# Kernel optimization log

Hardware: AMD Instinct MI355X
Metric: run time of the kernel (lower is better)

## Reference

```python
import jax, jax.numpy as jnp
import numpy as np

NUM_HEADS = 16
D_MODEL = 1024
DEPTH = D_MODEL // NUM_HEADS


def setup_inputs() -> dict:
    key = jax.random.key(0)
    ks = jax.random.split(key, 9)
    B, S = 2, 2048
    scale = 1.0 / np.sqrt(D_MODEL)
    return {
        "x": jax.random.normal(ks[0], (B, S, D_MODEL), dtype=jnp.float32),
        "wq": jax.random.normal(ks[1], (D_MODEL, D_MODEL), dtype=jnp.float32) * scale,
        "bq": jnp.zeros((D_MODEL,), dtype=jnp.float32),
        "wk": jax.random.normal(ks[2], (D_MODEL, D_MODEL), dtype=jnp.float32) * scale,
        "bk": jnp.zeros((D_MODEL,), dtype=jnp.float32),
        "wv": jax.random.normal(ks[3], (D_MODEL, D_MODEL), dtype=jnp.float32) * scale,
        "bv": jnp.zeros((D_MODEL,), dtype=jnp.float32),
        "wo": jax.random.normal(ks[4], (D_MODEL, D_MODEL), dtype=jnp.float32) * scale,
        "bo": jnp.zeros((D_MODEL,), dtype=jnp.float32),
    }


def _split_heads(t):
    # [B, S, D] -> [B, H, S, depth]
    B, S, _ = t.shape
    return t.reshape(B, S, NUM_HEADS, DEPTH).transpose(0, 2, 1, 3)


def reference(x, wq, bq, wk, bk, wv, bv, wo, bo):
    q = _split_heads(x @ wq + bq)  # [B,H,S,d]
    k = _split_heads(x @ wk + bk)
    v = _split_heads(x @ wv + bv)
    logits = jnp.einsum("bhqd,bhkd->bhqk", q, k) / jnp.sqrt(jnp.float32(DEPTH))
    attn = jax.nn.softmax(logits, axis=-1)  # [B,H,S,S]
    ctx = jnp.einsum("bhqk,bhkd->bhqd", attn, v)
    B, H, S, d = ctx.shape
    concat = ctx.transpose(0, 2, 1, 3).reshape(B, S, D_MODEL)
    out = concat @ wo + bo
    return out, attn
```

## Files before the change

### kernel.cpp

```cpp
#include <hip/hip_runtime.h>
#include <hip/hip_bf16.h>

#define SEQ 2048
#define BATCH 2
#define NH 16
#define DM 1024
#define DEPTH 64
#define MROWS (BATCH * SEQ)

typedef __attribute__((ext_vector_type(8))) short bf16x8;
typedef __attribute__((ext_vector_type(4))) float f32x4;

__device__ __forceinline__ float b2f(ushort u) {
    union { uint i; float f; } v; v.i = ((uint)u) << 16; return v.f;
}
__device__ __forceinline__ ushort f2b(float f) {
    __hip_bfloat16 h = __float2bfloat16(f);
    return *reinterpret_cast<ushort*>(&h);
}

__device__ __forceinline__ void gload_lds16(const void* g, void* l) {
    __builtin_amdgcn_global_load_lds((const __attribute__((address_space(1))) void*)g,
                                     (__attribute__((address_space(3))) void*)l, 16, 0, 0);
}

__global__ __launch_bounds__(256) void convert_f32_bf16(const float* __restrict__ in,
                                                        ushort* __restrict__ outp, int n4) {
    int i = blockIdx.x * 256 + threadIdx.x;
    if (i < n4) {
        const float4 v = ((const float4*)in)[i];
        ushort4 o;
        o.x = f2b(v.x); o.y = f2b(v.y); o.z = f2b(v.z); o.w = f2b(v.w);
        ((ushort4*)outp)[i] = o;
    }
}

__global__ __launch_bounds__(256) void transpose_convert4(const float* __restrict__ w0,
                                                          const float* __restrict__ w1,
                                                          const float* __restrict__ w2,
                                                          const float* __restrict__ w3,
                                                          ushort* __restrict__ WtBase) {
    __shared__ float tile[32][33];
    const int z = blockIdx.z;
    const float* W = (z == 0) ? w0 : (z == 1) ? w1 : (z == 2) ? w2 : w3;
    ushort* Wt = WtBase + (size_t)z * DM * DM;
    const int bx = blockIdx.x * 32;
    const int by = blockIdx.y * 32;
    const int tx = threadIdx.x & 31, ty = threadIdx.x >> 5;
#pragma unroll
    for (int i = 0; i < 32; i += 8)
        tile[ty + i][tx] = W[(size_t)(by + ty + i) * DM + bx + tx];
    __syncthreads();
#pragma unroll
    for (int i = 0; i < 32; i += 8)
        Wt[(size_t)(bx + ty + i) * DM + by + tx] = f2b(tile[tx][ty + i]);
}

__global__ __launch_bounds__(256) void gemm_qkv_mfma(const ushort* __restrict__ A,
                                                     const ushort* __restrict__ WtAll,
                                                     const float* __restrict__ bq,
                                                     const float* __restrict__ bk,
                                                     const float* __restrict__ bv,
                                                     ushort* __restrict__ OutBase) {
    __shared__ __align__(16) ushort As[128 * 32];
    __shared__ __align__(16) ushort Bs[128 * 32];

    const int t    = threadIdx.x;
    const int lane = t & 63;
    const int w    = t >> 6;
    const int wr   = w >> 1, wc = w & 1;
    const int row0 = blockIdx.y * 128;
    const int col0 = blockIdx.x * 128;
    const int bank = col0 >> 10;
    const float* bias = (bank == 0) ? bq : (bank == 1) ? bk : bv;
    const float scale = (bank == 0) ? 0.125f : 1.0f;
    const int ccol0 = col0 & 1023;
    ushort* Cout = OutBase + (size_t)bank * MROWS * DM;

    f32x4 acc[4][4];
#pragma unroll
    for (int mi = 0; mi < 4; ++mi)
#pragma unroll
        for (int ni = 0; ni < 4; ++ni) acc[mi][ni] = (f32x4){0.f, 0.f, 0.f, 0.f};

    const int sr = t >> 2;
    const int sc = (t & 3) * 8;

    for (int k0 = 0; k0 < DM; k0 += 32) {
        gload_lds16(&A[(size_t)(row0 + sr) * DM + k0 + sc],          &As[w * 512]);
        gload_lds16(&A[(size_t)(row0 + 64 + sr) * DM + k0 + sc],     &As[2048 + w * 512]);
        gload_lds16(&WtAll[(size_t)(col0 + sr) * DM + k0 + sc],      &Bs[w * 512]);
        gload_lds16(&WtAll[(size_t)(col0 + 64 + sr) * DM + k0 + sc], &Bs[2048 + w * 512]);
        __syncthreads();

        bf16x8 af[4], bfr[4];
#pragma unroll
        for (int mi = 0; mi < 4; ++mi)
            af[mi] = *(const bf16x8*)&As[(wr * 64 + mi * 16 + (lane & 15)) * 32 + (lane >> 4) * 8];
#pragma unroll
        for (int ni = 0; ni < 4; ++ni)
            bfr[ni] = *(const bf16x8*)&Bs[(wc * 64 + ni * 16 + (lane & 15)) * 32 + (lane >> 4) * 8];
#pragma unroll
        for (int mi = 0; mi < 4; ++mi)
#pragma unroll
            for (int ni = 0; ni < 4; ++ni)
                acc[mi][ni] = __builtin_amdgcn_mfma_f32_16x16x32_bf16(af[mi], bfr[ni], acc[mi][ni], 0, 0, 0);
        __syncthreads();
    }

    float bb[4];
#pragma unroll
    for (int ni = 0; ni < 4; ++ni) bb[ni] = bias[ccol0 + wc * 64 + ni * 16 + (lane & 15)];

#pragma unroll
    for (int mi = 0; mi < 4; ++mi) {
        const int row = row0 + wr * 64 + mi * 16 + (lane >> 4) * 4;
#pragma unroll
        for (int ni = 0; ni < 4; ++ni) {
            const int col = ccol0 + wc * 64 + ni * 16 + (lane & 15);
#pragma unroll
            for (int r = 0; r < 4; ++r)
                Cout[(size_t)(row + r) * DM + col] = f2b((acc[mi][ni][r] + bb[ni]) * scale);
        }
    }
}

__global__ __launch_bounds__(256) void gemm_mfma_f32(const ushort* __restrict__ A,
                                                     const ushort* __restrict__ Wt,
                                                     const float* __restrict__ bias,
                                                     float* __restrict__ Cout) {
    __shared__ __align__(16) ushort As[128 * 32];
    __shared__ __align__(16) ushort Bs[128 * 32];

    const int t    = threadIdx.x;
    const int lane = t & 63;
    const int w    = t >> 6;
    const int wr   = w >> 1, wc = w & 1;
    const int row0 = blockIdx.y * 128;
    const int col0 = blockIdx.x * 128;

    f32x4 acc[4][4];
#pragma unroll
    for (int mi = 0; mi < 4; ++mi)
#pragma unroll
        for (int ni = 0; ni < 4; ++ni) acc[mi][ni] = (f32x4){0.f, 0.f, 0.f, 0.f};

    const int sr = t >> 2;
    const int sc = (t & 3) * 8;

    for (int k0 = 0; k0 < DM; k0 += 32) {
        gload_lds16(&A[(size_t)(row0 + sr) * DM + k0 + sc],       &As[w * 512]);
        gload_lds16(&A[(size_t)(row0 + 64 + sr) * DM + k0 + sc],  &As[2048 + w * 512]);
        gload_lds16(&Wt[(size_t)(col0 + sr) * DM + k0 + sc],      &Bs[w * 512]);
        gload_lds16(&Wt[(size_t)(col0 + 64 + sr) * DM + k0 + sc], &Bs[2048 + w * 512]);
        __syncthreads();

        bf16x8 af[4], bfr[4];
#pragma unroll
        for (int mi = 0; mi < 4; ++mi)
            af[mi] = *(const bf16x8*)&As[(wr * 64 + mi * 16 + (lane & 15)) * 32 + (lane >> 4) * 8];
#pragma unroll
        for (int ni = 0; ni < 4; ++ni)
            bfr[ni] = *(const bf16x8*)&Bs[(wc * 64 + ni * 16 + (lane & 15)) * 32 + (lane >> 4) * 8];
#pragma unroll
        for (int mi = 0; mi < 4; ++mi)
#pragma unroll
            for (int ni = 0; ni < 4; ++ni)
                acc[mi][ni] = __builtin_amdgcn_mfma_f32_16x16x32_bf16(af[mi], bfr[ni], acc[mi][ni], 0, 0, 0);
        __syncthreads();
    }

    float bb[4];
#pragma unroll
    for (int ni = 0; ni < 4; ++ni) bb[ni] = bias[col0 + wc * 64 + ni * 16 + (lane & 15)];

#pragma unroll
    for (int mi = 0; mi < 4; ++mi) {
        const int row = row0 + wr * 64 + mi * 16 + (lane >> 4) * 4;
#pragma unroll
        for (int ni = 0; ni < 4; ++ni) {
            const int col = col0 + wc * 64 + ni * 16 + (lane & 15);
#pragma unroll
            for (int r = 0; r < 4; ++r)
                Cout[(size_t)(row + r) * DM + col] = acc[mi][ni][r] + bb[ni];
        }
    }
}

__global__ __launch_bounds__(256) void transpose_v(const ushort* __restrict__ Vh,
                                                   ushort* __restrict__ Vt3) {
    __shared__ ushort tile[64][80];
    const int t  = threadIdx.x;
    const int bh = blockIdx.x;
    const int cc = blockIdx.y;
    const int k0 = cc * 64;
    const int b  = bh >> 4;
    const int h  = bh & 15;
    const size_t panel = (size_t)b * SEQ * DM + (size_t)h * DEPTH;

    {
        const int k = t >> 2, dc = (t & 3) * 16;
        const ushort* src = Vh + panel + (size_t)(k0 + k) * DM + dc;
        *(bf16x8*)&tile[k][dc]     = *(const bf16x8*)src;
        *(bf16x8*)&tile[k][dc + 8] = *(const bf16x8*)(src + 8);
    }
    __syncthreads();
    {
        const int l  = t & 63;
        const int ni = t >> 6;
        const int kr = (l >> 4) * 8;
        const int dl = ni * 16 + (l & 15);
#pragma unroll
        for (int kh = 0; kh < 2; ++kh) {
            bf16x8 o;
#pragma unroll
            for (int j = 0; j < 8; ++j) o[j] = tile[kh * 32 + kr + j][dl];
            char* dst = (char*)Vt3 +
                        (((size_t)bh * 64 + cc * 2 + kh) * 4 + ni) * 1024 + l * 16;
            *(bf16x8*)dst = o;
        }
    }
}

__global__ __launch_bounds__(256) void transpose_k(const ushort* __restrict__ Kh,
                                                   ushort* __restrict__ Kf) {
    __shared__ ushort tile[64][80];
    const int t  = threadIdx.x;
    const int bh = blockIdx.x;
    const int cc = blockIdx.y;
    const int k0 = cc * 64;
    const int b  = bh >> 4;
    const int h  = bh & 15;
    const size_t panel = (size_t)b * SEQ * DM + (size_t)h * DEPTH;

    {
        const int k = t >> 2, dc = (t & 3) * 16;
        const ushort* src = Kh + panel + (size_t)(k0 + k) * DM + dc;
        *(bf16x8*)&tile[k][dc]     = *(const bf16x8*)src;
        *(bf16x8*)&tile[k][dc + 8] = *(const bf16x8*)(src + 8);
    }
    __syncthreads();
    {
        const int l   = t & 63;
        const int sub = t >> 6;
        const int row = sub * 16 + (l & 15);
        const int db  = (l >> 4) * 8;
#pragma unroll
        for (int ks = 0; ks < 2; ++ks) {
            bf16x8 o;
#pragma unroll
            for (int j = 0; j < 8; ++j) o[j] = tile[row][ks * 32 + db + j];
            char* dst = (char*)Kf +
                        ((((size_t)bh * 128 + cc * 4 + sub) * 2) + ks) * 1024 + l * 16;
            *(bf16x8*)dst = o;
        }
    }
}

__global__ __launch_bounds__(512, 2) void attn_fused_kernel(const ushort* __restrict__ Qh,
                                                            const ushort* __restrict__ Kfrag,
                                                            const ushort* __restrict__ Vt3,
                                                            float* __restrict__ attn_out,
                                                            ushort* __restrict__ Ctx) {
    __shared__ __align__(16) ushort P_lds[16 * 2048];
    __shared__ float red[256];

    const int t    = threadIdx.x;
    const int lane = t & 63;
    const int w    = t >> 6;
    const int qt   = blockIdx.x;
    const int bh   = blockIdx.y;
    const int b    = bh >> 4;
    const int h    = bh & 15;
    const int q0   = qt * 16;
    const int q    = lane & 15;
    const int g    = lane >> 4;
    const int swzP = (q & 7) << 4;

    const size_t panel = (size_t)b * SEQ * DM + (size_t)h * DEPTH;
    char* Pb = (char*)P_lds;

    const ushort* Qrow = Qh + panel + (size_t)(q0 + q) * DM + g * 8;
    const bf16x8 qf0 = *(const bf16x8*)Qrow;
    const bf16x8 qf1 = *(const bf16x8*)(Qrow + 32);

    const char* Kf = (const char*)Kfrag + (size_t)bh * 262144;
    f32x4 acc[16];
#pragma unroll
    for (int i = 0; i < 16; ++i) acc[i] = (f32x4){0.f, 0.f, 0.f, 0.f};

#pragma unroll
    for (int i = 0; i < 16; ++i) {
        const char* fb = Kf + (size_t)((w * 16 + i) * 2) * 1024 + lane * 16;
        const bf16x8 kf0 = *(const bf16x8*)fb;
        const bf16x8 kf1 = *(const bf16x8*)(fb + 1024);
        acc[i] = __builtin_amdgcn_mfma_f32_16x16x32_bf16(kf0, qf0, acc[i], 0, 0, 0);
        acc[i] = __builtin_amdgcn_mfma_f32_16x16x32_bf16(kf1, qf1, acc[i], 0, 0, 0);
    }

    float mm = acc[0][0];
#pragma unroll
    for (int i = 0; i < 16; ++i) {
#pragma unroll
        for (int r = 0; r < 4; ++r) mm = fmaxf(mm, acc[i][r]);
    }
    mm = fmaxf(mm, __shfl_xor(mm, 16));
    mm = fmaxf(mm, __shfl_xor(mm, 32));
    if (lane < 16) red[w * 16 + lane] = mm;
    __syncthreads();

    float mx = red[q];
#pragma unroll
    for (int ww = 1; ww < 8; ++ww) mx = fmaxf(mx, red[ww * 16 + q]);

    float ssum = 0.f;
#pragma unroll
    for (int i = 0; i < 16; ++i) {
#pragma unroll
        for (int r = 0; r < 4; ++r) {
            const float p = __expf(acc[i][r] - mx);
            acc[i][r] = p;
            ssum += p;
        }
    }
    ssum += __shfl_xor(ssum, 16);
    ssum += __shfl_xor(ssum, 32);
    if (lane < 16) red[128 + w * 16 + lane] = ssum;
    __syncthreads();

    float tot = red[128 + q];
#pragma unroll
    for (int ww = 1; ww < 8; ++ww) tot += red[128 + ww * 16 + q];
    const float rinv = 1.f / tot;

#pragma unroll
    for (int i = 0; i < 16; ++i) {
        const float p0 = acc[i][0] * rinv;
        const float p1 = acc[i][1] * rinv;
        const float p2 = acc[i][2] * rinv;
        const float p3 = acc[i][3] * rinv;
        uint2 uu;
        uu.x = (uint)f2b(p0) | ((uint)f2b(p1) << 16);
        uu.y = (uint)f2b(p2) | ((uint)f2b(p3) << 16);
        *(uint2*)(Pb + q * 4096 + ((w * 512 + i * 32 + g * 8) ^ swzP)) = uu;
    }
    __syncthreads();

    float* attn_base = attn_out + ((size_t)bh * SEQ + q0) * SEQ;
#pragma unroll
    for (int it = 0; it < 16; ++it) {
        const int bofs = (w * 512 + lane * 8) ^ ((it & 7) << 4);
        const ushort4 p4 = *(const ushort4*)(Pb + it * 4096 + bofs);
        f32x4 o;
        o[0] = b2f(p4.x); o[1] = b2f(p4.y); o[2] = b2f(p4.z); o[3] = b2f(p4.w);
        __builtin_nontemporal_store(o, (f32x4*)&attn_base[(size_t)it * SEQ + w * 256 + lane * 4]);
    }

    const char* Vf = (const char*)Vt3 + (size_t)bh * 262144;
    f32x4 ctx[4];
#pragma unroll
    for (int ni = 0; ni < 4; ++ni) ctx[ni] = (f32x4){0.f, 0.f, 0.f, 0.f};

#pragma unroll
    for (int s8 = 0; s8 < 8; ++s8) {
        const bf16x8 af = *(const bf16x8*)(Pb + q * 4096 + ((w * 512 + s8 * 64 + g * 16) ^ swzP));
        const char* fb = Vf + (size_t)((w * 8 + s8) * 4) * 1024 + lane * 16;
#pragma unroll
        for (int ni = 0; ni < 4; ++ni) {
            const bf16x8 bfr = *(const bf16x8*)(fb + ni * 1024);
            ctx[ni] = __builtin_amdgcn_mfma_f32_16x16x32_bf16(af, bfr, ctx[ni], 0, 0, 0);
        }
    }
    __syncthreads();

    float* part = (float*)P_lds;
#pragma unroll
    for (int ni = 0; ni < 4; ++ni) {
#pragma unroll
        for (int r = 0; r < 4; ++r) {
            part[(w * 16 + g * 4 + r) * 64 + ni * 16 + q] = ctx[ni][r];
        }
    }
    __syncthreads();

#pragma unroll
    for (int idx = t; idx < 1024; idx += 512) {
        const int qq = idx >> 6, d = idx & 63;
        float s2 = 0.f;
#pragma unroll
        for (int ww = 0; ww < 8; ++ww) s2 += part[ww * 1024 + idx];
        Ctx[(size_t)(b * SEQ + q0 + qq) * DM + h * DEPTH + d] = f2b(s2);
    }
}

extern "C" void kernel_launch(void* const* d_in, const int* in_sizes, int n_in,
                              void* d_out, int out_size, void* d_ws, size_t ws_size,
                              hipStream_t stream) {
    const float* x  = (const float*)d_in[0];
    const float* wq = (const float*)d_in[1];
    const float* bq = (const float*)d_in[2];
    const float* wk = (const float*)d_in[3];
    const float* bk = (const float*)d_in[4];
    const float* wv = (const float*)d_in[5];
    const float* bv = (const float*)d_in[6];
    const float* wo = (const float*)d_in[7];
    const float* bo = (const float*)d_in[8];

    float* out  = (float*)d_out;
    float* attn = out + (size_t)MROWS * DM;

    ushort* ws  = (ushort*)d_ws;
    ushort* xb  = ws;
    ushort* wqt = xb + (size_t)MROWS * DM;
    ushort* wot = wqt + (size_t)3 * DM * DM;
    ushort* Qh  = wot + (size_t)DM * DM;
    ushort* Kh  = Qh + (size_t)MROWS * DM;
    ushort* Vh  = Kh + (size_t)MROWS * DM;
    ushort* cxb = Vh + (size_t)MROWS * DM;
    ushort* Vt3 = cxb + (size_t)MROWS * DM;
    ushort* Kf  = Vt3 + (size_t)BATCH * NH * DEPTH * SEQ;

    convert_f32_bf16<<<dim3(MROWS * DM / 4 / 256), 256, 0, stream>>>(x, xb, MROWS * DM / 4);
    transpose_convert4<<<dim3(DM / 32, DM / 32, 4), 256, 0, stream>>>(wq, wk, wv, wo, wqt);

    gemm_qkv_mfma<<<dim3(3 * DM / 128, MROWS / 128), 256, 0, stream>>>(xb, wqt, bq, bk, bv, Qh);

    transpose_v<<<dim3(BATCH * NH, SEQ / 64), 256, 0, stream>>>(Vh, Vt3);
    transpose_k<<<dim3(BATCH * NH, SEQ / 64), 256, 0, stream>>>(Kh, Kf);

    attn_fused_kernel<<<dim3(SEQ / 16, BATCH * NH), 512, 0, stream>>>(Qh, Kf, Vt3, attn, cxb);

    gemm_mfma_f32<<<dim3(DM / 128, MROWS / 128), 256, 0, stream>>>(cxb, wot, bo, out);
}
```

Before: 219.8 us.

## Vectorize GEMM epilogues, merge K/V transposes, tree reductions and setprio in attention

Swaps the MFMA operands in both projection GEMMs so each lane holds four consecutive output columns, which allows vectorized bias loads and 8-byte or 16-byte output stores instead of scalar strided stores. Merges the separate K and V transpose kernels into one launch with a z-dimension selecting the mode, removing one launch. In the attention kernel it replaces serial max/sum chains with tree reductions for more ILP and raises wave priority around the MFMA loops. These are several unrelated micro-optimizations, and the epilogue layout change must keep the output indexing correct.

Result: slower. 231.2 us (+5.1%).

```diff
diff --git a/kernel.cpp b/kernel.cpp
--- a/kernel.cpp
+++ b/kernel.cpp
@@ -104,23 +104,23 @@
         for (int mi = 0; mi < 4; ++mi)
 #pragma unroll
             for (int ni = 0; ni < 4; ++ni)
-                acc[mi][ni] = __builtin_amdgcn_mfma_f32_16x16x32_bf16(af[mi], bfr[ni], acc[mi][ni], 0, 0, 0);
+                acc[mi][ni] = __builtin_amdgcn_mfma_f32_16x16x32_bf16(bfr[ni], af[mi], acc[mi][ni], 0, 0, 0);
         __syncthreads();
     }
 
-    float bb[4];
-#pragma unroll
-    for (int ni = 0; ni < 4; ++ni) bb[ni] = bias[ccol0 + wc * 64 + ni * 16 + (lane & 15)];
-
 #pragma unroll
     for (int mi = 0; mi < 4; ++mi) {
-        const int row = row0 + wr * 64 + mi * 16 + (lane >> 4) * 4;
+        const int seq = row0 + wr * 64 + mi * 16 + (lane & 15);
 #pragma unroll
         for (int ni = 0; ni < 4; ++ni) {
-            const int col = ccol0 + wc * 64 + ni * 16 + (lane & 15);
-#pragma unroll
-            for (int r = 0; r < 4; ++r)
-                Cout[(size_t)(row + r) * DM + col] = f2b((acc[mi][ni][r] + bb[ni]) * scale);
+            const int dbase = ccol0 + wc * 64 + ni * 16 + (lane >> 4) * 4;
+            const float4 b4 = *(const float4*)&bias[dbase];
+            ushort4 o;
+            o.x = f2b((acc[mi][ni][0] + b4.x) * scale);
+            o.y = f2b((acc[mi][ni][1] + b4.y) * scale);
+            o.z = f2b((acc[mi][ni][2] + b4.z) * scale);
+            o.w = f2b((acc[mi][ni][3] + b4.w) * scale);
+            *(ushort4*)&Cout[(size_t)seq * DM + dbase] = o;
         }
     }
 }
@@ -166,46 +166,65 @@
         for (int mi = 0; mi < 4; ++mi)
 #pragma unroll
             for (int ni = 0; ni < 4; ++ni)
-                acc[mi][ni] = __builtin_amdgcn_mfma_f32_16x16x32_bf16(af[mi], bfr[ni], acc[mi][ni], 0, 0, 0);
+                acc[mi][ni] = __builtin_amdgcn_mfma_f32_16x16x32_bf16(bfr[ni], af[mi], acc[mi][ni], 0, 0, 0);
         __syncthreads();
     }
 
-    float bb[4];
-#pragma unroll
-    for (int ni = 0; ni < 4; ++ni) bb[ni] = bias[col0 + wc * 64 + ni * 16 + (lane & 15)];
-
 #pragma unroll
     for (int mi = 0; mi < 4; ++mi) {
-        const int row = row0 + wr * 64 + mi * 16 + (lane >> 4) * 4;
+        const int seq = row0 + wr * 64 + mi * 16 + (lane & 15);
 #pragma unroll
         for (int ni = 0; ni < 4; ++ni) {
-            const int col = col0 + wc * 64 + ni * 16 + (lane & 15);
-#pragma unroll
-            for (int r = 0; r < 4; ++r)
-                Cout[(size_t)(row + r) * DM + col] = acc[mi][ni][r] + bb[ni];
-        }
-    }
-}
-
-__global__ __launch_bounds__(256) void transpose_v(const ushort* __restrict__ Vh,
-                                                   ushort* __restrict__ Vt3) {
+            const int dbase = col0 + wc * 64 + ni * 16 + (lane >> 4) * 4;
+            const float4 b4 = *(const float4*)&bias[dbase];
+            f32x4 o;
+            o[0] = acc[mi][ni][0] + b4.x;
+            o[1] = acc[mi][ni][1] + b4.y;
+            o[2] = acc[mi][ni][2] + b4.z;
+            o[3] = acc[mi][ni][3] + b4.w;
+            *(f32x4*)&Cout[(size_t)seq * DM + dbase] = o;
+        }
+    }
+}
+
+__global__ __launch_bounds__(256) void transpose_kv(const ushort* __restrict__ Kh,
+                                                    const ushort* __restrict__ Vh,
+                                                    ushort* __restrict__ Kf,
+                                                    ushort* __restrict__ Vt3) {
     __shared__ ushort tile[64][80];
-    const int t  = threadIdx.x;
-    const int bh = blockIdx.x;
-    const int cc = blockIdx.y;
-    const int k0 = cc * 64;
-    const int b  = bh >> 4;
-    const int h  = bh & 15;
+    const int t    = threadIdx.x;
+    const int bh   = blockIdx.x;
+    const int cc   = blockIdx.y;
+    const int mode = blockIdx.z;
+    const int k0   = cc * 64;
+    const int b    = bh >> 4;
+    const int h    = bh & 15;
     const size_t panel = (size_t)b * SEQ * DM + (size_t)h * DEPTH;
+    const ushort* S = mode ? Vh : Kh;
 
     {
         const int k = t >> 2, dc = (t & 3) * 16;
-        const ushort* src = Vh + panel + (size_t)(k0 + k) * DM + dc;
+        const ushort* src = S + panel + (size_t)(k0 + k) * DM + dc;
         *(bf16x8*)&tile[k][dc]     = *(const bf16x8*)src;
         *(bf16x8*)&tile[k][dc + 8] = *(const bf16x8*)(src + 8);
     }
     __syncthreads();
-    {
+
+    if (mode == 0) {
+        const int l   = t & 63;
+        const int sub = t >> 6;
+        const int row = sub * 16 + (l & 15);
+        const int db  = (l >> 4) * 8;
+#pragma unroll
+        for (int ks = 0; ks < 2; ++ks) {
+            bf16x8 o;
+#pragma unroll
+            for (int j = 0; j < 8; ++j) o[j] = tile[row][ks * 32 + db + j];
+            char* dst = (char*)Kf +
+                        ((((size_t)bh * 128 + cc * 4 + sub) * 2) + ks) * 1024 + l * 16;
+            *(bf16x8*)dst = o;
+        }
+    } else {
         const int l  = t & 63;
         const int ni = t >> 6;
         const int kr = (l >> 4) * 8;
@@ -217,41 +236,6 @@
             for (int j = 0; j < 8; ++j) o[j] = tile[kh * 32 + kr + j][dl];
             char* dst = (char*)Vt3 +
                         (((size_t)bh * 64 + cc * 2 + kh) * 4 + ni) * 1024 + l * 16;
-            *(bf16x8*)dst = o;
-        }
-    }
-}
-
-__global__ __launch_bounds__(256) void transpose_k(const ushort* __restrict__ Kh,
-                                                   ushort* __restrict__ Kf) {
-    __shared__ ushort tile[64][80];
-    const int t  = threadIdx.x;
-    const int bh = blockIdx.x;
-    const int cc = blockIdx.y;
-    const int k0 = cc * 64;
-    const int b  = bh >> 4;
-    const int h  = bh & 15;
-    const size_t panel = (size_t)b * SEQ * DM + (size_t)h * DEPTH;
-
-    {
-        const int k = t >> 2, dc = (t & 3) * 16;
-        const ushort* src = Kh + panel + (size_t)(k0 + k) * DM + dc;
-        *(bf16x8*)&tile[k][dc]     = *(const bf16x8*)src;
-        *(bf16x8*)&tile[k][dc + 8] = *(const bf16x8*)(src + 8);
-    }
-    __syncthreads();
-    {
-        const int l   = t & 63;
-        const int sub = t >> 6;
-        const int row = sub * 16 + (l & 15);
-        const int db  = (l >> 4) * 8;
-#pragma unroll
-        for (int ks = 0; ks < 2; ++ks) {
-            bf16x8 o;
-#pragma unroll
-            for (int j = 0; j < 8; ++j) o[j] = tile[row][ks * 32 + db + j];
-            char* dst = (char*)Kf +
-                        ((((size_t)bh * 128 + cc * 4 + sub) * 2) + ks) * 1024 + l * 16;
             *(bf16x8*)dst = o;
         }
     }
@@ -289,6 +273,7 @@
 #pragma unroll
     for (int i = 0; i < 16; ++i) acc[i] = (f32x4){0.f, 0.f, 0.f, 0.f};
 
+    __builtin_amdgcn_s_setprio(1);
 #pragma unroll
     for (int i = 0; i < 16; ++i) {
         const char* fb = Kf + (size_t)((w * 16 + i) * 2) * 1024 + lane * 16;
@@ -297,13 +282,17 @@
         acc[i] = __builtin_amdgcn_mfma_f32_16x16x32_bf16(kf0, qf0, acc[i], 0, 0, 0);
         acc[i] = __builtin_amdgcn_mfma_f32_16x16x32_bf16(kf1, qf1, acc[i], 0, 0, 0);
     }
-
-    float mm = acc[0][0];
-#pragma unroll
-    for (int i = 0; i < 16; ++i) {
-#pragma unroll
-        for (int r = 0; r < 4; ++r) mm = fmaxf(mm, acc[i][r]);
-    }
+    __builtin_amdgcn_s_setprio(0);
+
+    float pm[16];
+#pragma unroll
+    for (int i = 0; i < 16; ++i)
+        pm[i] = fmaxf(fmaxf(acc[i][0], acc[i][1]), fmaxf(acc[i][2], acc[i][3]));
+#pragma unroll
+    for (int s = 8; s > 0; s >>= 1)
+#pragma unroll
+        for (int i = 0; i < s; ++i) pm[i] = fmaxf(pm[i], pm[i + s]);
+    float mm = pm[0];
     mm = fmaxf(mm, __shfl_xor(mm, 16));
     mm = fmaxf(mm, __shfl_xor(mm, 32));
     if (lane < 16) red[w * 16 + lane] = mm;
@@ -313,16 +302,21 @@
 #pragma unroll
     for (int ww = 1; ww < 8; ++ww) mx = fmaxf(mx, red[ww * 16 + q]);
 
-    float ssum = 0.f;
+    float ps[16];
 #pragma unroll
     for (int i = 0; i < 16; ++i) {
-#pragma unroll
-        for (int r = 0; r < 4; ++r) {
-            const float p = __expf(acc[i][r] - mx);
-            acc[i][r] = p;
-            ssum += p;
-        }
-    }
+        const float e0 = __expf(acc[i][0] - mx);
+        const float e1 = __expf(acc[i][1] - mx);
+        const float e2 = __expf(acc[i][2] - mx);
+        const float e3 = __expf(acc[i][3] - mx);
+        acc[i][0] = e0; acc[i][1] = e1; acc[i][2] = e2; acc[i][3] = e3;
+        ps[i] = (e0 + e1) + (e2 + e3);
+    }
+#pragma unroll
+    for (int s = 8; s > 0; s >>= 1)
+#pragma unroll
+        for (int i = 0; i < s; ++i) ps[i] += ps[i + s];
+    float ssum = ps[0];
     ssum += __shfl_xor(ssum, 16);
     ssum += __shfl_xor(ssum, 32);
     if (lane < 16) red[128 + w * 16 + lane] = ssum;
@@ -361,6 +355,7 @@
 #pragma unroll
     for (int ni = 0; ni < 4; ++ni) ctx[ni] = (f32x4){0.f, 0.f, 0.f, 0.f};
 
+    __builtin_amdgcn_s_setprio(1);
 #pragma unroll
     for (int s8 = 0; s8 < 8; ++s8) {
         const bf16x8 af = *(const bf16x8*)(Pb + q * 4096 + ((w * 512 + s8 * 64 + g * 16) ^ swzP));
@@ -371,6 +366,7 @@
             ctx[ni] = __builtin_amdgcn_mfma_f32_16x16x32_bf16(af, bfr, ctx[ni], 0, 0, 0);
         }
     }
+    __builtin_amdgcn_s_setprio(0);
     __syncthreads();
 
     float* part = (float*)P_lds;
@@ -425,8 +421,7 @@
 
     gemm_qkv_mfma<<<dim3(3 * DM / 128, MROWS / 128), 256, 0, stream>>>(xb, wqt, bq, bk, bv, Qh);
 
-    transpose_v<<<dim3(BATCH * NH, SEQ / 64), 256, 0, stream>>>(Vh, Vt3);
-    transpose_k<<<dim3(BATCH * NH, SEQ / 64), 256, 0, stream>>>(Kh, Kf);
+    transpose_kv<<<dim3(BATCH * NH, SEQ / 64, 2), 256, 0, stream>>>(Kh, Vh, Kf, Vt3);
 
     attn_fused_kernel<<<dim3(SEQ / 16, BATCH * NH), 512, 0, stream>>>(Qh, Kf, Vt3, attn, cxb);
 
```
